# Kernel tuning notes

Measured on AMD Instinct MI355X. Metric: run time of the kernel, lower is better.

## Reference

```python
import jax, jax.numpy as jnp
import numpy as np

DIM = 1024          # BIGNET_DIM
LORA = 32
GROUP = 128
N_LIN = 18          # 6 blocks * 3 QLoRALinear
N_LN = 5
EPS = 1e-5


def setup_inputs() -> dict:
    key = jax.random.key(0)
    ks = jax.random.split(key, 8)
    tokens = 16384
    x = jax.random.normal(ks[0], (tokens, DIM), dtype=jnp.float32)
    # int4 codes in [0,16), per-(out,group) scale (block-abs-max norm)
    q = jax.random.randint(ks[1], (N_LIN, DIM, DIM), 0, 16, dtype=jnp.int32)
    norm = jax.random.uniform(ks[2], (N_LIN, DIM, DIM // GROUP), dtype=jnp.float32) * 0.1 + 0.01
    bias = jax.random.normal(ks[3], (N_LIN, DIM), dtype=jnp.float32) * 0.01
    # lora_a: kaiming-uniform * 0.01; lora_b: zeros in the original init, but we use
    # small random values so the LoRA path (and its gradients) are exercised.
    lora_a = jax.random.normal(ks[4], (N_LIN, LORA, DIM), dtype=jnp.float32) * 0.01
    lora_b = jax.random.normal(ks[5], (N_LIN, DIM, LORA), dtype=jnp.float32) * 0.01
    ln_gamma = jnp.ones((N_LN, DIM), dtype=jnp.float32)
    ln_beta = jnp.zeros((N_LN, DIM), dtype=jnp.float32)
    return {"x": x, "q": q, "norm": norm, "bias": bias,
            "lora_a": lora_a, "lora_b": lora_b,
            "ln_gamma": ln_gamma, "ln_beta": ln_beta}


def _dequant(qi, ni):
    # qi: [O, I] int codes in [0,16); ni: [O, I//GROUP] group scales
    O, I = qi.shape
    w = (qi.astype(jnp.float32) / 15.0 * 2.0 - 1.0).reshape(O, I // GROUP, GROUP)
    return (w * ni[..., None]).reshape(O, I)


def _qlora_linear(h, qi, ni, b, la, lb):
    w = _dequant(qi, ni)                      # [O, I]
    base = h @ w.T + b                        # frozen quantized path
    lora = (h @ la.T) @ lb.T                  # rank-32 adapter
    return base + lora


def _layernorm(h, g, b):
    mu = jnp.mean(h, axis=-1, keepdims=True)
    var = jnp.var(h, axis=-1, keepdims=True)
    return (h - mu) * jax.lax.rsqrt(var + EPS) * g + b


def _forward(x, q, norm, bias, lora_a, lora_b, ln_gamma, ln_beta):
    h = x
    for blk in range(6):
        r = h
        for j in range(3):
            i = 3 * blk + j
            r = _qlora_linear(r, q[i], norm[i], bias[i], lora_a[i], lora_b[i])
            if j < 2:
                r = jax.nn.relu(r)
        h = r + h                              # residual
        if blk < 5:
            h = _layernorm(h, ln_gamma[blk], ln_beta[blk])
    return h


def reference(x, q, norm, bias, lora_a, lora_b, ln_gamma, ln_beta):
    return _forward(x, q, norm, bias, lora_a, lora_b, ln_gamma, ln_beta)
```

## Files before the change

### kernel.cpp

```cpp
#include <hip/hip_runtime.h>
#include <stdint.h>


#define TOK   16384
#define DIM   1024
#define NLIN  18
#define EPS   1e-5f

typedef _Float16 f16;
typedef _Float16 f16x8 __attribute__((ext_vector_type(8)));
typedef _Float16 f16x4 __attribute__((ext_vector_type(4)));
typedef float    f32x4 __attribute__((ext_vector_type(4)));

__device__ __forceinline__ void load_lds16(const void* g, void* l) {
  __builtin_amdgcn_global_load_lds(
      (const __attribute__((address_space(1))) void*)g,
      (__attribute__((address_space(3))) void*)l,
      16, 0, 0);
}

__global__ __launch_bounds__(256) void prep_w2(
    const int* __restrict__ q, const float* __restrict__ norm,
    const float* __restrict__ la, const float* __restrict__ lb,
    f16* __restrict__ W)
{
  __shared__ float lbs[128 * 32];
  const int bid   = blockIdx.x;
  const int i     = bid >> 5;
  const int ot    = (bid >> 2) & 7;
  const int ktile = bid & 3;
  const int o0 = ot * 128, k0 = ktile * 256;
  const int tid = threadIdx.x;
  const int kg = tid & 63, og = tid >> 6;
  const int k4 = k0 + kg * 4;

  const float* lbsrc = lb + (size_t)i * DIM * 32 + (size_t)o0 * 32;
  #pragma unroll
  for (int p = 0; p < 4; ++p)
    *(float4*)(lbs + p * 1024 + tid * 4) = *(const float4*)(lbsrc + p * 1024 + tid * 4);

  float4 lar[32];
  const float* lasrc = la + (size_t)i * 32 * DIM + k4;
  #pragma unroll
  for (int r = 0; r < 32; ++r) lar[r] = *(const float4*)(lasrc + r * DIM);
  __syncthreads();

  const float s = 2.f / 15.f;
  for (int oi = 0; oi < 32; ++oi) {
    const int o = o0 + og * 32 + oi;
    const size_t wb = ((size_t)i * DIM + o) * DIM;
    const int4 qv = *(const int4*)(q + wb + k4);
    const float nrm = norm[((size_t)i * DIM + o) * 8 + (k4 >> 7)];
    const float* lbr = lbs + (og * 32 + oi) * 32;
    float ax = 0.f, ay = 0.f, az = 0.f, aw = 0.f;
    #pragma unroll
    for (int r = 0; r < 32; ++r) {
      const float b = lbr[r];
      ax += b * lar[r].x; ay += b * lar[r].y; az += b * lar[r].z; aw += b * lar[r].w;
    }
    f16x4 hv;
    hv[0] = (f16)(((float)qv.x * s - 1.f) * nrm + ax);
    hv[1] = (f16)(((float)qv.y * s - 1.f) * nrm + ay);
    hv[2] = (f16)(((float)qv.z * s - 1.f) * nrm + az);
    hv[3] = (f16)(((float)qv.w * s - 1.f) * nrm + aw);
    *(f16x4*)(W + wb + k4) = hv;
  }
}

__global__ __launch_bounds__(256) void cvt_x(
    const float* __restrict__ x, f16* __restrict__ o)
{
  const size_t idx = ((size_t)blockIdx.x * 256 + threadIdx.x) * 4;
  const float4 v = *(const float4*)(x + idx);
  f16x4 h;
  h[0] = (f16)v.x; h[1] = (f16)v.y; h[2] = (f16)v.z; h[3] = (f16)v.w;
  *(f16x4*)(o + idx) = h;
}

#define BARX() __builtin_amdgcn_s_barrier()

#define RD_AF(afd, sl, kk) do { \
  _Pragma("unroll") \
  for (int mi = 0; mi < 8; ++mi) \
    afd[mi] = *(const f16x8*)(smem + (sl) + wmbase + arowb[mi] + (ckA ^ ((kk) << 6))); \
} while (0)

#define RD_BF(b0, b1, sl, np, kk) do { \
  b0 = *(const f16x8*)(smem + (sl) + 32768 + wnhalf + browb[(np)*2]     + (ckA ^ ((kk) << 6))); \
  b1 = *(const f16x8*)(smem + (sl) + 32768 + wnhalf + browb[(np)*2 + 1] + (ckA ^ ((kk) << 6))); \
} while (0)

#define QUAD(afr, b0, b1, nn) do { \
  __builtin_amdgcn_s_setprio(1); \
  _Pragma("unroll") \
  for (int mi = 0; mi < 8; ++mi) { \
    acc[mi][nn]     = __builtin_amdgcn_mfma_f32_16x16x32_f16(afr[mi], b0, acc[mi][nn],     0, 0, 0); \
    acc[mi][(nn)+1] = __builtin_amdgcn_mfma_f32_16x16x32_f16(afr[mi], b1, acc[mi][(nn)+1], 0, 0, 0); \
  } \
  __builtin_amdgcn_s_setprio(0); \
} while (0)

#define STAGE_A(T, h, dslot) do { \
  load_lds16(gA + (size_t)((T) * 64) + (size_t)((h) * 128) * DIM, \
             smem + (dslot) + (h) * 16384 + sdst); \
  load_lds16(gA + (size_t)((T) * 64) + (size_t)((h) * 128 + 64) * DIM, \
             smem + (dslot) + (h) * 16384 + 8192 + sdst); \
} while (0)
#define STAGE_B(T, h, dslot) do { \
  load_lds16(gB + (size_t)((T) * 64) + (size_t)((h) * 128) * DIM, \
             smem + (dslot) + 32768 + (h) * 16384 + sdst); \
  load_lds16(gB + (size_t)((T) * 64) + (size_t)((h) * 128 + 64) * DIM, \
             smem + (dslot) + 32768 + (h) * 16384 + 8192 + sdst); \
} while (0)

template<int EPI>
__global__ __launch_bounds__(512, 2) void gemm4(
    const f16* __restrict__ A, const f16* __restrict__ W,
    const float* __restrict__ bias, const f16* __restrict__ resid,
    void* __restrict__ outp)
{
  __shared__ __align__(16) char smem[131072];

  const int orig = blockIdx.x;
  const int swzb = (orig & 7) * 32 + (orig >> 3);
  const int mt = swzb >> 2, nt = swzb & 3;
  const int t0 = mt * 256, n0 = nt * 256;

  const int tid  = threadIdx.x;
  const int lane = tid & 63;
  const int wid  = tid >> 6;
  const int wm = wid >> 2, wn = wid & 3;

  const int srow = tid >> 3;
  const int sch  = (tid & 7) ^ (srow & 7);
  const f16* gA = A + (size_t)(t0 + srow) * DIM + sch * 8;
  const f16* gB = W + (size_t)(n0 + srow) * DIM + sch * 8;
  const int sdst = tid * 16;

  const int ckA    = (((lane >> 4) ^ (lane & 7)) << 4);
  const int wmbase = wm * 16384;
  const int wnhalf = (wn >> 1) * 16384;
  int arowb[8], browb[4];
  #pragma unroll
  for (int mi = 0; mi < 8; ++mi)
    arowb[mi] = (mi * 16 + (lane & 15)) * 128;
  #pragma unroll
  for (int ni = 0; ni < 4; ++ni)
    browb[ni] = ((wn & 1) * 64 + ni * 16 + (lane & 15)) * 128;

  f32x4 acc[8][4] = {};
  f16x8 afX[8], afY[8];
  f16x8 bfP0, bfP1, bfQ0, bfQ1, bfP20, bfP21, bfQ20, bfQ21;

  STAGE_A(0, 0, 0); STAGE_A(0, 1, 0);
  STAGE_B(0, 0, 0); STAGE_B(0, 1, 0);
  STAGE_A(1, 0, 65536); STAGE_A(1, 1, 65536);
  asm volatile("s_waitcnt vmcnt(4)" ::: "memory");
  BARX();
  RD_AF(afX, 0, 0);
  RD_BF(bfP0, bfP1, 0, 0, 0);

  for (int t = 0; t < 16; ++t) {
    const int sl = (t & 1) << 16;
    const int ns = sl ^ 65536;
    RD_BF(bfQ0, bfQ1, sl, 1, 0);
    if (t < 15) STAGE_B(t + 1, 0, ns);
    BARX();
    QUAD(afX, bfP0, bfP1, 0);
    RD_AF(afY, sl, 1);
    RD_BF(bfP20, bfP21, sl, 0, 1);
    if (t < 15) STAGE_B(t + 1, 1, ns);
    BARX();
    QUAD(afX, bfQ0, bfQ1, 2);
    RD_BF(bfQ20, bfQ21, sl, 1, 1);
    if (t < 14) STAGE_A(t + 2, 0, sl);
    BARX();
    QUAD(afY, bfP20, bfP21, 0);
    if (t < 14) {
      STAGE_A(t + 2, 1, sl);
      asm volatile("s_waitcnt vmcnt(2)" ::: "memory");
    } else {
      asm volatile("s_waitcnt vmcnt(0)" ::: "memory");
    }
    BARX();
    if (t < 15) {
      RD_AF(afX, ns, 0);
      RD_BF(bfP0, bfP1, ns, 0, 0);
    }
    QUAD(afY, bfQ20, bfQ21, 2);
  }

  const int colb = lane & 15;
  const int rowb = (lane >> 4) << 2;
  #pragma unroll
  for (int ni = 0; ni < 4; ++ni) {
    const int col = n0 + wn * 64 + ni * 16 + colb;
    const float bv = bias[col];
    #pragma unroll
    for (int mi = 0; mi < 8; ++mi) {
      const int trow = t0 + wm * 128 + mi * 16 + rowb;
      const f32x4 v = acc[mi][ni];
      #pragma unroll
      for (int r = 0; r < 4; ++r) {
        const size_t idx = (size_t)(trow + r) * DIM + col;
        float val = v[r] + bv;
        if constexpr (EPI == 0) {
          val = fmaxf(val, 0.f);
          ((f16*)outp)[idx] = (f16)val;
        } else if constexpr (EPI == 1) {
          val += (float)resid[idx];
          ((f16*)outp)[idx] = (f16)val;
        } else {
          val += (float)resid[idx];
          ((float*)outp)[idx] = val;
        }
      }
    }
  }
}

__global__ __launch_bounds__(256) void ln_k(
    const f16* __restrict__ in, f16* __restrict__ out,
    const float* __restrict__ g, const float* __restrict__ b)
{
  __shared__ float red[8];
  const int row = blockIdx.x;
  const int tid = threadIdx.x;
  const int c = tid * 4;
  const f16x4 v4 = *(const f16x4*)(in + (size_t)row * DIM + c);
  const float v0 = v4[0], v1 = v4[1], v2 = v4[2], v3 = v4[3];
  float s  = v0 + v1 + v2 + v3;
  float s2 = v0 * v0 + v1 * v1 + v2 * v2 + v3 * v3;
  #pragma unroll
  for (int off = 32; off; off >>= 1) {
    s  += __shfl_xor(s,  off);
    s2 += __shfl_xor(s2, off);
  }
  if ((tid & 63) == 0) { red[(tid >> 6) * 2] = s; red[(tid >> 6) * 2 + 1] = s2; }
  __syncthreads();
  s  = red[0] + red[2] + red[4] + red[6];
  s2 = red[1] + red[3] + red[5] + red[7];
  const float mu  = s * (1.f / DIM);
  const float var = fmaxf(s2 * (1.f / DIM) - mu * mu, 0.f);
  const float rs  = rsqrtf(var + EPS);
  const float4 gv = *(const float4*)(g + c);
  const float4 bv = *(const float4*)(b + c);
  f16x4 o4;
  o4[0] = (f16)((v0 - mu) * rs * gv.x + bv.x);
  o4[1] = (f16)((v1 - mu) * rs * gv.y + bv.y);
  o4[2] = (f16)((v2 - mu) * rs * gv.z + bv.z);
  o4[3] = (f16)((v3 - mu) * rs * gv.w + bv.w);
  *(f16x4*)(out + (size_t)row * DIM + c) = o4;
}

extern "C" void kernel_launch(void* const* d_in, const int* in_sizes, int n_in,
                              void* d_out, int out_size, void* d_ws, size_t ws_size,
                              hipStream_t stream)
{
  (void)in_sizes; (void)n_in; (void)out_size; (void)ws_size;
  const float* x     = (const float*)d_in[0];
  const int*   q     = (const int*)d_in[1];
  const float* norm  = (const float*)d_in[2];
  const float* bias  = (const float*)d_in[3];
  const float* la    = (const float*)d_in[4];
  const float* lb    = (const float*)d_in[5];
  const float* lg    = (const float*)d_in[6];
  const float* lbeta = (const float*)d_in[7];

  char* ws = (char*)d_ws;
  f16* W    = (f16*)ws;
  f16* buf1 = (f16*)(ws + (size_t)NLIN * DIM * DIM * 2);
  f16* buf2 = buf1 + (size_t)TOK * DIM;
  f16* buf0 = (f16*)d_out;
  f16* bufs[3] = {buf0, buf1, buf2};

  prep_w2<<<NLIN * 32, 256, 0, stream>>>(q, norm, la, lb, W);
  cvt_x<<<TOK * DIM / 1024, 256, 0, stream>>>(x, buf0);

  int h = 0;
  for (int blk = 0; blk < 6; ++blk) {
    const int a = (h == 0) ? 1 : 0;
    const int p = 3 - h - a;
    const int i0 = blk * 3;
    const size_t wsz = (size_t)DIM * DIM;
    gemm4<0><<<256, 512, 0, stream>>>(bufs[h], W + (i0 + 0) * wsz,
                                      bias + (i0 + 0) * DIM, nullptr, bufs[a]);
    gemm4<0><<<256, 512, 0, stream>>>(bufs[a], W + (i0 + 1) * wsz,
                                      bias + (i0 + 1) * DIM, nullptr, bufs[p]);
    if (blk < 5) {
      gemm4<1><<<256, 512, 0, stream>>>(bufs[p], W + (i0 + 2) * wsz,
                                        bias + (i0 + 2) * DIM, bufs[h], bufs[a]);
      ln_k<<<TOK, 256, 0, stream>>>(bufs[a], bufs[a], lg + blk * DIM, lbeta + blk * DIM);
      h = a;
    } else {
      gemm4<2><<<256, 512, 0, stream>>>(bufs[p], W + (i0 + 2) * wsz,
                                        bias + (i0 + 2) * DIM, bufs[h], d_out);
    }
  }
}
```

Baseline: 981.6 us.

## Restructure GEMM main loop: load all fragments up front, finer MFMA quads

Replaces the interleaved fragment-read and MFMA schedule with a ping-pong loop. Each K-tile's A and B register fragments (both k halves) are read into registers at once, then the MFMAs run in four quarter groups with more barriers between them. The LDS layout now keeps separate A and B double-buffer regions, and the global-to-LDS staging of the next A and B tiles is spread across the quarters. This is meant to cut LDS read stalls and overlap the loads more evenly with compute. The cost is a higher fragment register footprint and many more barriers per iteration.

Measured after the change: 1.082 ms. 1.1x slower.

```diff
diff --git a/kernel.cpp b/kernel.cpp
--- a/kernel.cpp
+++ b/kernel.cpp
@@ -78,43 +78,58 @@
 }
 
 #define BARX() __builtin_amdgcn_s_barrier()
-
-#define RD_AF(afd, sl, kk) do { \
-  _Pragma("unroll") \
-  for (int mi = 0; mi < 8; ++mi) \
-    afd[mi] = *(const f16x8*)(smem + (sl) + wmbase + arowb[mi] + (ckA ^ ((kk) << 6))); \
+#define SA0 0
+#define SA1 32768
+#define SB0 65536
+#define SB1 98304
+
+#define LDA(sa, mi, kk) (*(const f16x8*)(smem + (sa) + wmbase + arowb[mi] + (ckA ^ ((kk) << 6))))
+#define LDB(sb, ni, kk) (*(const f16x8*)(smem + (sb) + wnhalf + browb[ni] + (ckA ^ ((kk) << 6))))
+
+#define RD_ALL(sa, sb) do { \
+  af[0][0] = LDA(sa, 0, 0); af[0][1] = LDA(sa, 0, 1); \
+  af[1][0] = LDA(sa, 1, 0); af[1][1] = LDA(sa, 1, 1); \
+  bf[0][0] = LDB(sb, 0, 0); bf[0][1] = LDB(sb, 0, 1); \
+  bf[1][0] = LDB(sb, 1, 0); bf[1][1] = LDB(sb, 1, 1); \
+  bf[2][0] = LDB(sb, 2, 0); bf[2][1] = LDB(sb, 2, 1); \
+  bf[3][0] = LDB(sb, 3, 0); bf[3][1] = LDB(sb, 3, 1); \
+  af[2][0] = LDA(sa, 2, 0); af[2][1] = LDA(sa, 2, 1); \
+  af[3][0] = LDA(sa, 3, 0); af[3][1] = LDA(sa, 3, 1); \
+  af[4][0] = LDA(sa, 4, 0); af[4][1] = LDA(sa, 4, 1); \
+  af[5][0] = LDA(sa, 5, 0); af[5][1] = LDA(sa, 5, 1); \
+  af[6][0] = LDA(sa, 6, 0); af[6][1] = LDA(sa, 6, 1); \
+  af[7][0] = LDA(sa, 7, 0); af[7][1] = LDA(sa, 7, 1); \
 } while (0)
 
-#define RD_BF(b0, b1, sl, np, kk) do { \
-  b0 = *(const f16x8*)(smem + (sl) + 32768 + wnhalf + browb[(np)*2]     + (ckA ^ ((kk) << 6))); \
-  b1 = *(const f16x8*)(smem + (sl) + 32768 + wnhalf + browb[(np)*2 + 1] + (ckA ^ ((kk) << 6))); \
-} while (0)
-
-#define QUAD(afr, b0, b1, nn) do { \
+#define QUADQ(q) do { \
   __builtin_amdgcn_s_setprio(1); \
   _Pragma("unroll") \
-  for (int mi = 0; mi < 8; ++mi) { \
-    acc[mi][nn]     = __builtin_amdgcn_mfma_f32_16x16x32_f16(afr[mi], b0, acc[mi][nn],     0, 0, 0); \
-    acc[mi][(nn)+1] = __builtin_amdgcn_mfma_f32_16x16x32_f16(afr[mi], b1, acc[mi][(nn)+1], 0, 0, 0); \
+  for (int ni = 0; ni < 4; ++ni) { \
+    acc[2*(q)][ni]   = __builtin_amdgcn_mfma_f32_16x16x32_f16(af[2*(q)][0],   bf[ni][0], acc[2*(q)][ni],   0, 0, 0); \
+    acc[2*(q)][ni]   = __builtin_amdgcn_mfma_f32_16x16x32_f16(af[2*(q)][1],   bf[ni][1], acc[2*(q)][ni],   0, 0, 0); \
+    acc[2*(q)+1][ni] = __builtin_amdgcn_mfma_f32_16x16x32_f16(af[2*(q)+1][0], bf[ni][0], acc[2*(q)+1][ni], 0, 0, 0); \
+    acc[2*(q)+1][ni] = __builtin_amdgcn_mfma_f32_16x16x32_f16(af[2*(q)+1][1], bf[ni][1], acc[2*(q)+1][ni], 0, 0, 0); \
   } \
   __builtin_amdgcn_s_setprio(0); \
 } while (0)
 
-#define STAGE_A(T, h, dslot) do { \
+#define STAGE_A(T, h, base) do { \
   load_lds16(gA + (size_t)((T) * 64) + (size_t)((h) * 128) * DIM, \
-             smem + (dslot) + (h) * 16384 + sdst); \
+             smem + (base) + (h) * 16384 + sdst); \
   load_lds16(gA + (size_t)((T) * 64) + (size_t)((h) * 128 + 64) * DIM, \
-             smem + (dslot) + (h) * 16384 + 8192 + sdst); \
+             smem + (base) + (h) * 16384 + 8192 + sdst); \
 } while (0)
-#define STAGE_B(T, h, dslot) do { \
+#define STAGE_B(T, h, base) do { \
   load_lds16(gB + (size_t)((T) * 64) + (size_t)((h) * 128) * DIM, \
-             smem + (dslot) + 32768 + (h) * 16384 + sdst); \
+             smem + (base) + (h) * 16384 + sdst); \
   load_lds16(gB + (size_t)((T) * 64) + (size_t)((h) * 128 + 64) * DIM, \
-             smem + (dslot) + 32768 + (h) * 16384 + 8192 + sdst); \
+             smem + (base) + (h) * 16384 + 8192 + sdst); \
 } while (0)
 
+#define VMC(n) asm volatile("s_waitcnt vmcnt(" #n ")" ::: "memory")
+
 template<int EPI>
-__global__ __launch_bounds__(512, 2) void gemm4(
+__global__ __launch_bounds__(512, 2) void gemm5(
     const f16* __restrict__ A, const f16* __restrict__ W,
     const float* __restrict__ bias, const f16* __restrict__ resid,
     void* __restrict__ outp)
@@ -149,45 +164,35 @@
     browb[ni] = ((wn & 1) * 64 + ni * 16 + (lane & 15)) * 128;
 
   f32x4 acc[8][4] = {};
-  f16x8 afX[8], afY[8];
-  f16x8 bfP0, bfP1, bfQ0, bfQ1, bfP20, bfP21, bfQ20, bfQ21;
-
-  STAGE_A(0, 0, 0); STAGE_A(0, 1, 0);
-  STAGE_B(0, 0, 0); STAGE_B(0, 1, 0);
-  STAGE_A(1, 0, 65536); STAGE_A(1, 1, 65536);
-  asm volatile("s_waitcnt vmcnt(4)" ::: "memory");
+  f16x8 af[8][2], bf[4][2];
+
+  STAGE_A(0, 0, SA0); STAGE_A(0, 1, SA0);
+  STAGE_B(0, 0, SB0); STAGE_B(0, 1, SB0);
+  STAGE_B(1, 0, SB1); STAGE_B(1, 1, SB1);
+  VMC(4);
   BARX();
-  RD_AF(afX, 0, 0);
-  RD_BF(bfP0, bfP1, 0, 0, 0);
-
-  for (int t = 0; t < 16; ++t) {
-    const int sl = (t & 1) << 16;
-    const int ns = sl ^ 65536;
-    RD_BF(bfQ0, bfQ1, sl, 1, 0);
-    if (t < 15) STAGE_B(t + 1, 0, ns);
-    BARX();
-    QUAD(afX, bfP0, bfP1, 0);
-    RD_AF(afY, sl, 1);
-    RD_BF(bfP20, bfP21, sl, 0, 1);
-    if (t < 15) STAGE_B(t + 1, 1, ns);
-    BARX();
-    QUAD(afX, bfQ0, bfQ1, 2);
-    RD_BF(bfQ20, bfQ21, sl, 1, 1);
-    if (t < 14) STAGE_A(t + 2, 0, sl);
-    BARX();
-    QUAD(afY, bfP20, bfP21, 0);
-    if (t < 14) {
-      STAGE_A(t + 2, 1, sl);
-      asm volatile("s_waitcnt vmcnt(2)" ::: "memory");
-    } else {
-      asm volatile("s_waitcnt vmcnt(0)" ::: "memory");
-    }
-    BARX();
-    if (t < 15) {
-      RD_AF(afX, ns, 0);
-      RD_BF(bfP0, bfP1, ns, 0, 0);
-    }
-    QUAD(afY, bfQ20, bfQ21, 2);
+
+  for (int it = 0; it < 8; ++it) {
+    const int u = it * 2;
+    RD_ALL(SA0, SB0);
+    if (u + 1 < 16) STAGE_A(u + 1, 0, SA1);
+    BARX(); QUADQ(0); BARX();
+    if (u + 1 < 16) STAGE_A(u + 1, 1, SA1);
+    BARX(); QUADQ(1); BARX();
+    if (u + 2 < 16) STAGE_B(u + 2, 0, SB0);
+    BARX(); QUADQ(2); BARX();
+    if (u + 2 < 16) { STAGE_B(u + 2, 1, SB0); VMC(4); }
+    else            { VMC(0); }
+    BARX(); QUADQ(3); BARX();
+    RD_ALL(SA1, SB1);
+    if (u + 2 < 16) STAGE_A(u + 2, 0, SA0);
+    BARX(); QUADQ(0); BARX();
+    if (u + 2 < 16) STAGE_A(u + 2, 1, SA0);
+    BARX(); QUADQ(1); BARX();
+    if (u + 3 < 16) STAGE_B(u + 3, 0, SB1);
+    BARX(); QUADQ(2); BARX();
+    if (u + 3 < 16) { STAGE_B(u + 3, 1, SB1); VMC(4); }
+    BARX(); QUADQ(3); BARX();
   }
 
   const int colb = lane & 15;
@@ -283,17 +288,17 @@
     const int p = 3 - h - a;
     const int i0 = blk * 3;
     const size_t wsz = (size_t)DIM * DIM;
-    gemm4<0><<<256, 512, 0, stream>>>(bufs[h], W + (i0 + 0) * wsz,
+    gemm5<0><<<256, 512, 0, stream>>>(bufs[h], W + (i0 + 0) * wsz,
                                       bias + (i0 + 0) * DIM, nullptr, bufs[a]);
-    gemm4<0><<<256, 512, 0, stream>>>(bufs[a], W + (i0 + 1) * wsz,
+    gemm5<0><<<256, 512, 0, stream>>>(bufs[a], W + (i0 + 1) * wsz,
                                       bias + (i0 + 1) * DIM, nullptr, bufs[p]);
     if (blk < 5) {
-      gemm4<1><<<256, 512, 0, stream>>>(bufs[p], W + (i0 + 2) * wsz,
+      gemm5<1><<<256, 512, 0, stream>>>(bufs[p], W + (i0 + 2) * wsz,
                                         bias + (i0 + 2) * DIM, bufs[h], bufs[a]);
       ln_k<<<TOK, 256, 0, stream>>>(bufs[a], bufs[a], lg + blk * DIM, lbeta + blk * DIM);
       h = a;
     } else {
-      gemm4<2><<<256, 512, 0, stream>>>(bufs[p], W + (i0 + 2) * wsz,
+      gemm5<2><<<256, 512, 0, stream>>>(bufs[p], W + (i0 + 2) * wsz,
                                         bias + (i0 + 2) * DIM, bufs[h], d_out);
     }
   }
```
